# Performance work log

Hardware: AMD Instinct MI355X
Metric: run time of the kernel (lower is better)

## Reference

```python
import jax, jax.numpy as jnp
import numpy as np

N_NODES = 100000


def gcn_conv(x, edge_index, W, b):
    # PyG GCNConv: linear first, then symmetric-normalized aggregation with self-loops, then bias.
    n = x.shape[0]
    h = x @ W  # [N, out]
    loop = jnp.arange(n, dtype=edge_index.dtype)
    src = jnp.concatenate([edge_index[0], loop])  # source nodes (x_j)
    dst = jnp.concatenate([edge_index[1], loop])  # target nodes (aggregation index)
    ones = jnp.ones(dst.shape[0], dtype=h.dtype)
    deg = jax.ops.segment_sum(ones, dst, num_segments=n)  # in-degree incl. self-loop
    dinv = jnp.where(deg > 0, jax.lax.rsqrt(deg), 0.0)
    norm = dinv[src] * dinv[dst]  # [E+N]
    msgs = h[src] * norm[:, None]  # gather + scale
    out = jax.ops.segment_sum(msgs, dst, num_segments=n)  # scatter-add
    return out + b


def setup_inputs() -> dict:
    key = jax.random.key(0)
    k1, k2, k3, k4 = jax.random.split(key, 4)
    x = jax.random.normal(k1, (N_NODES, 128), dtype=jnp.float32)
    edge_index = jax.random.randint(k2, (2, 3200000), 0, N_NODES, dtype=jnp.int64)
    W1 = jax.random.normal(k3, (128, 16), dtype=jnp.float32) * (1.0 / np.sqrt(128))
    b1 = jnp.zeros((16,), dtype=jnp.float32)
    W2 = jax.random.normal(k4, (16, 10), dtype=jnp.float32) * (1.0 / np.sqrt(16))
    b2 = jnp.zeros((10,), dtype=jnp.float32)
    return {"x": x, "edge_index": edge_index, "W1": W1, "b1": b1, "W2": W2, "b2": b2}


def reference(x, edge_index, W1, b1, W2, b2):
    h = gcn_conv(x, edge_index, W1, b1)
    h = jax.nn.relu(h)
    h = gcn_conv(h, edge_index, W2, b2)
    return jax.nn.log_softmax(h, axis=1)
```

## Files before the change

kernel.cpp:

```cpp
#include <hip/hip_runtime.h>
#include <hip/hip_fp16.h>
#include <math.h>

#define NN 100000
#define F0 128
#define F1 16
#define F2 10
#define NBUCK 391
#define MAXB 10240
#define TILE 8192
#define EPT 16
#define CAP 10240
#define BPT 512

__device__ inline void fma4(float4& a, float s, const float4& w) {
  a.x = fmaf(s, w.x, a.x);
  a.y = fmaf(s, w.y, a.y);
  a.z = fmaf(s, w.z, a.z);
  a.w = fmaf(s, w.w, a.w);
}

__device__ inline unsigned pk2(float a, float b) {
  __half ha = __float2half(a), hb = __float2half(b);
  return (unsigned)__half_as_ushort(ha) | ((unsigned)__half_as_ushort(hb) << 16);
}

__device__ inline float2 up2(unsigned u) {
  __half2 h;
  *(unsigned*)&h = u;
  return __half22float2(h);
}

__device__ inline void nt_store_f2(float a, float b, float* p) {
  union { double d; float f[2]; } u;
  u.f[0] = a; u.f[1] = b;
  __builtin_nontemporal_store(u.d, (double*)p);
}

__global__ void k_zero(int* __restrict__ bucket_cur) {
  int i = blockIdx.x * blockDim.x + threadIdx.x;
  if (i < NBUCK) bucket_cur[i] = 0;
}

__global__ __launch_bounds__(BPT) void k_binplace(const int* __restrict__ src,
                                                  const int* __restrict__ dst, int E,
                                                  int* __restrict__ bucket_cur,
                                                  int* __restrict__ packed) {
  __shared__ int cnt[NBUCK];
  __shared__ int loff[NBUCK];
  __shared__ int gbase[NBUCK];
  __shared__ int part[256];
  __shared__ int stage[TILE];
  int t = threadIdx.x;
  int e0 = blockIdx.x * TILE, e1 = min(E, e0 + TILE);
  int total = e1 - e0;
  for (int i = t; i < NBUCK; i += BPT) cnt[i] = 0;
  __syncthreads();
  int bkpos[EPT];
  int pval[EPT];
#pragma unroll
  for (int k = 0; k < EPT; k++) {
    int e = e0 + t + k * BPT;
    if (e < e1) {
      int d = __builtin_nontemporal_load(dst + e);
      int s = __builtin_nontemporal_load(src + e);
      int bk = d >> 8;
      int pos = atomicAdd(&cnt[bk], 1);
      bkpos[k] = (bk << 13) | pos;
      pval[k] = (s << 8) | (d & 255);
    } else {
      bkpos[k] = -1;
    }
  }
  __syncthreads();
  for (int i = t; i < NBUCK; i += BPT) {
    int c = cnt[i];
    gbase[i] = c ? atomicAdd(&bucket_cur[i], c) : 0;
  }
  if (t < 256) {
    int i0 = 2 * t, i1 = 2 * t + 1;
    int c0 = (i0 < NBUCK) ? cnt[i0] : 0;
    int c1 = (i1 < NBUCK) ? cnt[i1] : 0;
    part[t] = c0 + c1;
  }
  __syncthreads();
  for (int o = 1; o < 256; o <<= 1) {
    int add = 0;
    if (t < 256 && t >= o) add = part[t - o];
    __syncthreads();
    if (t < 256) part[t] += add;
    __syncthreads();
  }
  if (t < 256) {
    int i0 = 2 * t, i1 = 2 * t + 1;
    int c0 = (i0 < NBUCK) ? cnt[i0] : 0;
    int c1 = (i1 < NBUCK) ? cnt[i1] : 0;
    int excl = part[t] - c0 - c1;
    if (i0 < NBUCK) loff[i0] = excl;
    if (i1 < NBUCK) loff[i1] = excl + c0;
  }
  __syncthreads();
#pragma unroll
  for (int k = 0; k < EPT; k++) {
    if (bkpos[k] >= 0) {
      int bk = bkpos[k] >> 13, pos = bkpos[k] & 8191;
      stage[loff[bk] + pos] = pval[k];
    }
  }
  __syncthreads();
  int sub = t >> 4, lane = t & 15;
  for (int bk = sub; bk < NBUCK; bk += BPT / 16) {
    int lo = loff[bk];
    int hi = (bk + 1 < NBUCK) ? loff[bk + 1] : total;
    size_t gb = (size_t)bk * MAXB + gbase[bk];
    for (int i = lo + lane; i < hi; i += 16) packed[gb + (i - lo)] = stage[i];
  }
}

__global__ __launch_bounds__(256) void k_bucket(const int* __restrict__ packed,
                                                const int* __restrict__ bucket_cur,
                                                int* __restrict__ row_start,
                                                int* __restrict__ row_end,
                                                float* __restrict__ dinv,
                                                int* __restrict__ col) {
  __shared__ int stage[CAP];
  __shared__ unsigned short posa[CAP];
  __shared__ int hist[256];
  __shared__ int offx[256];
  __shared__ int scan[256];
  __shared__ int cur[256];
  int b = blockIdx.x, t = threadIdx.x;
  size_t base = (size_t)b * MAXB;
  int cnt_b = bucket_cur[b];
  hist[t] = 0;
  __syncthreads();
  bool staged = (cnt_b <= CAP);
  if (staged) {
    for (int i = t; i < cnt_b; i += 256) {
      int p = __builtin_nontemporal_load(packed + base + i);
      stage[i] = p;
      int pos = atomicAdd(&hist[p & 255], 1);
      posa[i] = (unsigned short)pos;
    }
  } else {
    for (int i = t; i < cnt_b; i += 256)
      atomicAdd(&hist[packed[base + i] & 255], 1);
  }
  __syncthreads();
  int v = hist[t];
  scan[t] = v;
  __syncthreads();
  for (int o = 1; o < 256; o <<= 1) {
    int add = (t >= o) ? scan[t - o] : 0;
    __syncthreads();
    scan[t] += add;
    __syncthreads();
  }
  int excl = scan[t] - v;
  offx[t] = excl;
  cur[t] = excl;
  int d = b * 256 + t;
  if (d < NN) {
    row_start[d] = (int)base + excl;
    row_end[d] = (int)base + excl + v;
    dinv[d] = rsqrtf((float)(v + 1));
  }
  __syncthreads();
  if (staged) {
    for (int i = t; i < cnt_b; i += 256) {
      int p = stage[i];
      col[base + offx[p & 255] + posa[i]] = p >> 8;
    }
  } else {
    for (int i = t; i < cnt_b; i += 256) {
      int p = packed[base + i];
      int pos = atomicAdd(&cur[p & 255], 1);
      col[base + pos] = p >> 8;
    }
  }
}

__global__ __launch_bounds__(256) void k_lin1(const float* __restrict__ x,
                                              const float* __restrict__ W1,
                                              const float* __restrict__ dinv,
                                              unsigned* __restrict__ tab1) {
  __shared__ float4 wl[F0 * 4];
  int t = threadIdx.x;
  for (int i = t; i < F0 * 4; i += 256) wl[i] = ((const float4*)W1)[i];
  __syncthreads();
  int row0 = (blockIdx.x * 256 + t) * 4;
  if (row0 >= NN) return;
  float4 acc[4][4];
#pragma unroll
  for (int r = 0; r < 4; r++)
#pragma unroll
    for (int j = 0; j < 4; j++) acc[r][j] = make_float4(0.f, 0.f, 0.f, 0.f);
  const float4* xr0 = (const float4*)(x + (size_t)(row0 + 0) * F0);
  const float4* xr1 = (const float4*)(x + (size_t)(row0 + 1) * F0);
  const float4* xr2 = (const float4*)(x + (size_t)(row0 + 2) * F0);
  const float4* xr3 = (const float4*)(x + (size_t)(row0 + 3) * F0);
  for (int k4 = 0; k4 < F0 / 4; k4++) {
    float4 xv[4];
    xv[0] = xr0[k4]; xv[1] = xr1[k4]; xv[2] = xr2[k4]; xv[3] = xr3[k4];
#pragma unroll
    for (int kk = 0; kk < 4; kk++) {
      float4 w0 = wl[(k4 * 4 + kk) * 4 + 0];
      float4 w1 = wl[(k4 * 4 + kk) * 4 + 1];
      float4 w2 = wl[(k4 * 4 + kk) * 4 + 2];
      float4 w3 = wl[(k4 * 4 + kk) * 4 + 3];
#pragma unroll
      for (int r = 0; r < 4; r++) {
        float xs = kk == 0 ? xv[r].x : kk == 1 ? xv[r].y : kk == 2 ? xv[r].z : xv[r].w;
        fma4(acc[r][0], xs, w0);
        fma4(acc[r][1], xs, w1);
        fma4(acc[r][2], xs, w2);
        fma4(acc[r][3], xs, w3);
      }
    }
  }
#pragma unroll
  for (int r = 0; r < 4; r++) {
    float dd = dinv[row0 + r];
    float4 a0 = acc[r][0], a1 = acc[r][1], a2 = acc[r][2], a3 = acc[r][3];
    uint4 o0, o1;
    o0.x = pk2(dd * a0.x, dd * a0.y);
    o0.y = pk2(dd * a0.z, dd * a0.w);
    o0.z = pk2(dd * a1.x, dd * a1.y);
    o0.w = pk2(dd * a1.z, dd * a1.w);
    o1.x = pk2(dd * a2.x, dd * a2.y);
    o1.y = pk2(dd * a2.z, dd * a2.w);
    o1.z = pk2(dd * a3.x, dd * a3.y);
    o1.w = pk2(dd * a3.z, dd * a3.w);
    uint4* orow = (uint4*)(tab1 + (size_t)(row0 + r) * 8);
    orow[0] = o0;
    orow[1] = o1;
  }
}

__global__ __launch_bounds__(256) void k_agg1(const unsigned* __restrict__ tab1,
                                              const int* __restrict__ row_start,
                                              const int* __restrict__ row_end,
                                              const int* __restrict__ col,
                                              const float* __restrict__ dinv,
                                              const float* __restrict__ b1,
                                              const float* __restrict__ W2g,
                                              unsigned* __restrict__ tab2) {
  __shared__ float w2[F1][F2];
  __shared__ float b1l[F1];
  int t = threadIdx.x;
  if (t < F1 * F2) w2[t / F2][t % F2] = W2g[t];
  if (t < F1) b1l[t] = b1[t];
  __syncthreads();
  int g = blockIdx.x * 256 + t;
  int d = g >> 3, o = g & 7;
  int q2 = o >> 2, q = o & 3;
  if (d >= NN) return;
  const uint2* T = (const uint2*)tab1;
  float a0 = 0.f, a1 = 0.f, a2 = 0.f, a3 = 0.f;
  auto addrow = [&](int s) {
    uint2 v = T[(size_t)s * 4 + q];
    float2 f0 = up2(v.x), f1 = up2(v.y);
    a0 += f0.x; a1 += f0.y; a2 += f1.x; a3 += f1.y;
  };
  if (q2 == 0) addrow(d);
  int e = row_start[d] + q2, e1 = row_end[d];
  for (; e + 6 < e1; e += 8) {
    int s0 = __builtin_nontemporal_load(col + e);
    int s1 = __builtin_nontemporal_load(col + e + 2);
    int s2 = __builtin_nontemporal_load(col + e + 4);
    int s3 = __builtin_nontemporal_load(col + e + 6);
    addrow(s0); addrow(s1); addrow(s2); addrow(s3);
  }
  for (; e < e1; e += 2) addrow(__builtin_nontemporal_load(col + e));
  a0 += __shfl_xor(a0, 4);
  a1 += __shfl_xor(a1, 4);
  a2 += __shfl_xor(a2, 4);
  a3 += __shfl_xor(a3, 4);
  float dd = dinv[d];
  float h[4];
  h[0] = fmaxf(fmaf(dd, a0, b1l[q * 4 + 0]), 0.f);
  h[1] = fmaxf(fmaf(dd, a1, b1l[q * 4 + 1]), 0.f);
  h[2] = fmaxf(fmaf(dd, a2, b1l[q * 4 + 2]), 0.f);
  h[3] = fmaxf(fmaf(dd, a3, b1l[q * 4 + 3]), 0.f);
  float p[F2];
#pragma unroll
  for (int j = 0; j < F2; j++) {
    float s = 0.f;
#pragma unroll
    for (int kk = 0; kk < 4; kk++) s = fmaf(h[kk], w2[q * 4 + kk][j], s);
    p[j] = s;
  }
#pragma unroll
  for (int j = 0; j < F2; j++) p[j] += __shfl_xor(p[j], 1);
#pragma unroll
  for (int j = 0; j < F2; j++) p[j] += __shfl_xor(p[j], 2);
  if (q2 != 0) return;
  uint2* O = (uint2*)tab2;
  uint2 ov;
  if (q == 0) {
    ov.x = pk2(dd * p[0], dd * p[1]); ov.y = pk2(dd * p[2], dd * p[3]);
  } else if (q == 1) {
    ov.x = pk2(dd * p[4], dd * p[5]); ov.y = pk2(dd * p[6], dd * p[7]);
  } else if (q == 2) {
    ov.x = pk2(dd * p[8], dd * p[9]); ov.y = 0u;
  } else {
    ov.x = 0u; ov.y = 0u;
  }
  O[(size_t)d * 4 + q] = ov;
}

__global__ __launch_bounds__(256) void k_agg2(const unsigned* __restrict__ tab2,
                                              const int* __restrict__ row_start,
                                              const int* __restrict__ row_end,
                                              const int* __restrict__ col,
                                              const float* __restrict__ dinv,
                                              const float* __restrict__ b2,
                                              float* __restrict__ out) {
  __shared__ float b2l[F1];
  int t = threadIdx.x;
  if (t < F1) b2l[t] = (t < F2) ? b2[t] : -1e30f;
  __syncthreads();
  int g = blockIdx.x * 256 + t;
  int d = g >> 3, o = g & 7;
  int q2 = o >> 2, q = o & 3;
  if (d >= NN) return;
  const uint2* T = (const uint2*)tab2;
  float a0 = 0.f, a1 = 0.f, a2 = 0.f, a3 = 0.f;
  auto addrow = [&](int s) {
    uint2 v = T[(size_t)s * 4 + q];
    float2 f0 = up2(v.x), f1 = up2(v.y);
    a0 += f0.x; a1 += f0.y; a2 += f1.x; a3 += f1.y;
  };
  if (q2 == 0) addrow(d);
  int e = row_start[d] + q2, e1 = row_end[d];
  for (; e + 6 < e1; e += 8) {
    int s0 = __builtin_nontemporal_load(col + e);
    int s1 = __builtin_nontemporal_load(col + e + 2);
    int s2 = __builtin_nontemporal_load(col + e + 4);
    int s3 = __builtin_nontemporal_load(col + e + 6);
    addrow(s0); addrow(s1); addrow(s2); addrow(s3);
  }
  for (; e < e1; e += 2) addrow(__builtin_nontemporal_load(col + e));
  a0 += __shfl_xor(a0, 4);
  a1 += __shfl_xor(a1, 4);
  a2 += __shfl_xor(a2, 4);
  a3 += __shfl_xor(a3, 4);
  float dd = dinv[d];
  float v0 = fmaf(dd, a0, b2l[q * 4 + 0]);
  float v1 = fmaf(dd, a1, b2l[q * 4 + 1]);
  float v2 = fmaf(dd, a2, b2l[q * 4 + 2]);
  float v3 = fmaf(dd, a3, b2l[q * 4 + 3]);
  float m = fmaxf(fmaxf(v0, v1), fmaxf(v2, v3));
  m = fmaxf(m, __shfl_xor(m, 1));
  m = fmaxf(m, __shfl_xor(m, 2));
  float sum = expf(v0 - m) + expf(v1 - m) + expf(v2 - m) + expf(v3 - m);
  sum += __shfl_xor(sum, 1);
  sum += __shfl_xor(sum, 2);
  float lse = m + logf(sum);
  if (q2 != 0) return;
  float* op = out + (size_t)d * F2;
  if (q == 0) {
    nt_store_f2(v0 - lse, v1 - lse, op + 0);
    nt_store_f2(v2 - lse, v3 - lse, op + 2);
  } else if (q == 1) {
    nt_store_f2(v0 - lse, v1 - lse, op + 4);
    nt_store_f2(v2 - lse, v3 - lse, op + 6);
  } else if (q == 2) {
    nt_store_f2(v0 - lse, v1 - lse, op + 8);
  }
}

extern "C" void kernel_launch(void* const* d_in, const int* in_sizes, int n_in,
                              void* d_out, int out_size, void* d_ws, size_t ws_size,
                              hipStream_t stream) {
  const float* x  = (const float*)d_in[0];
  const int*   ei = (const int*)d_in[1];
  const float* W1 = (const float*)d_in[2];
  const float* b1 = (const float*)d_in[3];
  const float* W2 = (const float*)d_in[4];
  const float* b2 = (const float*)d_in[5];
  float* out = (float*)d_out;
  int E = in_sizes[1] / 2;
  const int* src = ei;
  const int* dst = ei + E;

  char* p = (char*)d_ws;
  auto alloc = [&](size_t bytes) {
    char* r = p;
    p += (bytes + 255) & ~(size_t)255;
    return r;
  };
  size_t tabsz = (size_t)NN * 8 * 4;
  size_t padded = (size_t)NBUCK * MAXB * 4;
  float* dinv       = (float*)alloc((size_t)NN * 4);
  int*   row_start  = (int*)alloc((size_t)NN * 4);
  int*   row_end    = (int*)alloc((size_t)NN * 4);
  int*   bucket_cur = (int*)alloc((size_t)NBUCK * 4);
  int*   col        = (int*)alloc(padded);
  size_t needA = tabsz * 2 > padded ? tabsz * 2 : padded;
  char*  A = (char*)alloc(needA);
  int*      packed = (int*)A;
  unsigned* tab1 = (unsigned*)A;
  unsigned* tab2 = (unsigned*)(A + tabsz);

  int nblk8N = (8 * NN + 255) / 256;
  int nblk_place = (E + TILE - 1) / TILE;
  hipLaunchKernelGGL(k_zero, dim3(2), dim3(256), 0, stream, bucket_cur);
  hipLaunchKernelGGL(k_binplace, dim3(nblk_place), dim3(BPT), 0, stream, src, dst, E, bucket_cur, packed);
  hipLaunchKernelGGL(k_bucket, dim3(NBUCK), dim3(256), 0, stream,
                     packed, bucket_cur, row_start, row_end, dinv, col);
  hipLaunchKernelGGL(k_lin1, dim3((NN / 4 + 255) / 256), dim3(256), 0, stream, x, W1, dinv, tab1);
  hipLaunchKernelGGL(k_agg1, dim3(nblk8N), dim3(256), 0, stream,
                     tab1, row_start, row_end, col, dinv, b1, W2, tab2);
  hipLaunchKernelGGL(k_agg2, dim3(nblk8N), dim3(256), 0, stream,
                     tab2, row_start, row_end, col, dinv, b2, out);
}
```

Baseline: 171.7 us.

## Stage x rows in LDS for lin1 and halve binplace tile size

```diff
diff --git a/kernel.cpp b/kernel.cpp
--- a/kernel.cpp
+++ b/kernel.cpp
@@ -8,17 +8,11 @@
 #define F2 10
 #define NBUCK 391
 #define MAXB 10240
-#define TILE 8192
-#define EPT 16
+#define TILE 4096
+#define EPT 8
 #define CAP 10240
 #define BPT 512
-
-__device__ inline void fma4(float4& a, float s, const float4& w) {
-  a.x = fmaf(s, w.x, a.x);
-  a.y = fmaf(s, w.y, a.y);
-  a.z = fmaf(s, w.z, a.z);
-  a.w = fmaf(s, w.w, a.w);
-}
+#define L1R 64
 
 __device__ inline unsigned pk2(float a, float b) {
   __half ha = __float2half(a), hb = __float2half(b);
@@ -66,7 +60,7 @@
       int s = __builtin_nontemporal_load(src + e);
       int bk = d >> 8;
       int pos = atomicAdd(&cnt[bk], 1);
-      bkpos[k] = (bk << 13) | pos;
+      bkpos[k] = (bk << 12) | pos;
       pval[k] = (s << 8) | (d & 255);
     } else {
       bkpos[k] = -1;
@@ -103,7 +97,7 @@
 #pragma unroll
   for (int k = 0; k < EPT; k++) {
     if (bkpos[k] >= 0) {
-      int bk = bkpos[k] >> 13, pos = bkpos[k] & 8191;
+      int bk = bkpos[k] >> 12, pos = bkpos[k] & 4095;
       stage[loff[bk] + pos] = pval[k];
     }
   }
@@ -185,56 +179,38 @@
                                               const float* __restrict__ dinv,
                                               unsigned* __restrict__ tab1) {
   __shared__ float4 wl[F0 * 4];
+  __shared__ float4 xs[L1R * 33];
   int t = threadIdx.x;
   for (int i = t; i < F0 * 4; i += 256) wl[i] = ((const float4*)W1)[i];
-  __syncthreads();
-  int row0 = (blockIdx.x * 256 + t) * 4;
-  if (row0 >= NN) return;
-  float4 acc[4][4];
-#pragma unroll
-  for (int r = 0; r < 4; r++)
-#pragma unroll
-    for (int j = 0; j < 4; j++) acc[r][j] = make_float4(0.f, 0.f, 0.f, 0.f);
-  const float4* xr0 = (const float4*)(x + (size_t)(row0 + 0) * F0);
-  const float4* xr1 = (const float4*)(x + (size_t)(row0 + 1) * F0);
-  const float4* xr2 = (const float4*)(x + (size_t)(row0 + 2) * F0);
-  const float4* xr3 = (const float4*)(x + (size_t)(row0 + 3) * F0);
-  for (int k4 = 0; k4 < F0 / 4; k4++) {
-    float4 xv[4];
-    xv[0] = xr0[k4]; xv[1] = xr1[k4]; xv[2] = xr2[k4]; xv[3] = xr3[k4];
-#pragma unroll
-    for (int kk = 0; kk < 4; kk++) {
-      float4 w0 = wl[(k4 * 4 + kk) * 4 + 0];
-      float4 w1 = wl[(k4 * 4 + kk) * 4 + 1];
-      float4 w2 = wl[(k4 * 4 + kk) * 4 + 2];
-      float4 w3 = wl[(k4 * 4 + kk) * 4 + 3];
-#pragma unroll
-      for (int r = 0; r < 4; r++) {
-        float xs = kk == 0 ? xv[r].x : kk == 1 ? xv[r].y : kk == 2 ? xv[r].z : xv[r].w;
-        fma4(acc[r][0], xs, w0);
-        fma4(acc[r][1], xs, w1);
-        fma4(acc[r][2], xs, w2);
-        fma4(acc[r][3], xs, w3);
-      }
-    }
-  }
-#pragma unroll
-  for (int r = 0; r < 4; r++) {
-    float dd = dinv[row0 + r];
-    float4 a0 = acc[r][0], a1 = acc[r][1], a2 = acc[r][2], a3 = acc[r][3];
-    uint4 o0, o1;
-    o0.x = pk2(dd * a0.x, dd * a0.y);
-    o0.y = pk2(dd * a0.z, dd * a0.w);
-    o0.z = pk2(dd * a1.x, dd * a1.y);
-    o0.w = pk2(dd * a1.z, dd * a1.w);
-    o1.x = pk2(dd * a2.x, dd * a2.y);
-    o1.y = pk2(dd * a2.z, dd * a2.w);
-    o1.z = pk2(dd * a3.x, dd * a3.y);
-    o1.w = pk2(dd * a3.z, dd * a3.w);
-    uint4* orow = (uint4*)(tab1 + (size_t)(row0 + r) * 8);
-    orow[0] = o0;
-    orow[1] = o1;
-  }
+  int row0 = blockIdx.x * L1R;
+  int nrows = min(L1R, NN - row0);
+  const float4* xg = (const float4*)(x + (size_t)row0 * F0);
+  for (int i = t; i < nrows * 32; i += 256) {
+    int rr = i >> 5, cc = i & 31;
+    xs[rr * 33 + cc] = xg[i];
+  }
+  __syncthreads();
+  int r = t >> 2, q = t & 3;
+  if (r >= nrows) return;
+  int d = row0 + r;
+  float4 acc = make_float4(0.f, 0.f, 0.f, 0.f);
+#pragma unroll
+  for (int k4 = 0; k4 < 32; k4++) {
+    float4 xv = xs[r * 33 + k4];
+    float4 w0 = wl[(k4 * 4 + 0) * 4 + q];
+    float4 w1 = wl[(k4 * 4 + 1) * 4 + q];
+    float4 w2 = wl[(k4 * 4 + 2) * 4 + q];
+    float4 w3 = wl[(k4 * 4 + 3) * 4 + q];
+    acc.x = fmaf(xv.x, w0.x, fmaf(xv.y, w1.x, fmaf(xv.z, w2.x, fmaf(xv.w, w3.x, acc.x))));
+    acc.y = fmaf(xv.x, w0.y, fmaf(xv.y, w1.y, fmaf(xv.z, w2.y, fmaf(xv.w, w3.y, acc.y))));
+    acc.z = fmaf(xv.x, w0.z, fmaf(xv.y, w1.z, fmaf(xv.z, w2.z, fmaf(xv.w, w3.z, acc.z))));
+    acc.w = fmaf(xv.x, w0.w, fmaf(xv.y, w1.w, fmaf(xv.z, w2.w, fmaf(xv.w, w3.w, acc.w))));
+  }
+  float dd = dinv[d];
+  uint2 o;
+  o.x = pk2(dd * acc.x, dd * acc.y);
+  o.y = pk2(dd * acc.z, dd * acc.w);
+  ((uint2*)tab1)[(size_t)d * 4 + q] = o;
 }
 
 __global__ __launch_bounds__(256) void k_agg1(const unsigned* __restrict__ tab1,
@@ -405,11 +381,12 @@
 
   int nblk8N = (8 * NN + 255) / 256;
   int nblk_place = (E + TILE - 1) / TILE;
+  int nblk_lin1 = (NN + L1R - 1) / L1R;
   hipLaunchKernelGGL(k_zero, dim3(2), dim3(256), 0, stream, bucket_cur);
   hipLaunchKernelGGL(k_binplace, dim3(nblk_place), dim3(BPT), 0, stream, src, dst, E, bucket_cur, packed);
   hipLaunchKernelGGL(k_bucket, dim3(NBUCK), dim3(256), 0, stream,
                      packed, bucket_cur, row_start, row_end, dinv, col);
-  hipLaunchKernelGGL(k_lin1, dim3((NN / 4 + 255) / 256), dim3(256), 0, stream, x, W1, dinv, tab1);
+  hipLaunchKernelGGL(k_lin1, dim3(nblk_lin1), dim3(256), 0, stream, x, W1, dinv, tab1);
   hipLaunchKernelGGL(k_agg1, dim3(nblk8N), dim3(256), 0, stream,
                      tab1, row_start, row_end, col, dinv, b1, W2, tab2);
   hipLaunchKernelGGL(k_agg2, dim3(nblk8N), dim3(256), 0, stream,
```

Result: faster. 164.0 us (-4.5%).
